# Performance work log

Hardware: AMD Instinct MI355X
Metric: run time of the kernel (lower is better)

## Reference

```python
import jax, jax.numpy as jnp
import numpy as np

WS = 8       # window_size
SHIFT = 4    # shift_size
HEADS = 4

def _rel_pos_index():
    coords = np.stack(np.meshgrid(np.arange(WS), np.arange(WS), indexing='ij'))
    cf = coords.reshape(2, -1)                       # (2, N)
    rel = cf[:, :, None] - cf[:, None, :]            # (2, N, N)
    rel = rel.transpose(1, 2, 0).copy()              # (N, N, 2)
    rel[:, :, 0] += WS - 1
    rel[:, :, 1] += WS - 1
    rel[:, :, 0] *= 2 * WS - 1
    return jnp.asarray(rel.sum(-1))                  # (N, N) int

REL_IDX = _rel_pos_index()

def _conv(x, w, groups=1, pad=0):
    return jax.lax.conv_general_dilated(
        x, w, (1, 1), [(pad, pad), (pad, pad)],
        feature_group_count=groups,
        dimension_numbers=('NCHW', 'OIHW', 'NCHW'))

def _dwt_haar(x):
    # single-level orthonormal Haar on non-overlapping 2x2 blocks
    B, C, H, W = x.shape
    x = x.reshape(B, C, H // 2, 2, W // 2, 2)
    a = x[:, :, :, 0, :, 0]; b = x[:, :, :, 0, :, 1]
    c = x[:, :, :, 1, :, 0]; d = x[:, :, :, 1, :, 1]
    ll = (a + b + c + d) * 0.5
    lh = (a - b + c - d) * 0.5
    hl = (a + b - c - d) * 0.5
    hh = (a - b - c + d) * 0.5
    return ll, lh, hl, hh

def _idwt_haar(ll, lh, hl, hh):
    a = (ll + lh + hl + hh) * 0.5
    b = (ll - lh + hl - hh) * 0.5
    c = (ll + lh - hl - hh) * 0.5
    d = (ll - lh - hl + hh) * 0.5
    B, C, H2, W2 = ll.shape
    x = jnp.stack([jnp.stack([a, b], -1), jnp.stack([c, d], -1)], -2)  # (B,C,H2,W2,2row,2col)
    return x.transpose(0, 1, 2, 4, 3, 5).reshape(B, C, 2 * H2, 2 * W2)

def _window_partition(x):
    B, C, H, W = x.shape
    x = x.reshape(B, C, H // WS, WS, W // WS, WS).transpose(0, 2, 4, 1, 3, 5)
    return x.reshape(-1, C, WS, WS)

def _window_reverse(w, B, H, W):
    C = w.shape[1]
    x = w.reshape(B, H // WS, W // WS, C, WS, WS).transpose(0, 3, 1, 4, 2, 5)
    return x.reshape(B, C, H, W)

def setup_inputs() -> dict:
    key = jax.random.key(0)
    ks = jax.random.split(key, 8)
    dim = 64
    s = 0.05
    return {
        'x': jax.random.normal(ks[0], (8, dim, 256, 256), jnp.float32),
        'temperature': jnp.ones((HEADS, 1, 1), jnp.float32),
        'rel_bias_table': jax.random.normal(ks[1], ((2 * WS - 1) ** 2, HEADS), jnp.float32) * 0.02,
        'w_high1': jax.random.normal(ks[2], (2 * dim, dim, 3, 3), jnp.float32) * s,
        'w_high2': jax.random.normal(ks[3], (dim, 2 * dim, 1, 1), jnp.float32) * s,
        'w_highout': jax.random.normal(ks[4], (3 * dim, dim, 3, 3), jnp.float32) * s,
        'w_qkv': jax.random.normal(ks[5], (3 * dim, dim, 1, 1), jnp.float32) * s,
        'w_dwconv': jax.random.normal(ks[6], (3 * dim, 1, 3, 3), jnp.float32) * s,
        'w_proj': jax.random.normal(ks[7], (dim, dim, 1, 1), jnp.float32) * s,
    }

def reference(x, temperature, rel_bias_table, w_high1, w_high2, w_highout, w_qkv, w_dwconv, w_proj):
    B, C, H, W = x.shape
    ll, lh, hl, hh = _dwt_haar(x)
    # high-frequency modulation of v
    filt = jax.nn.relu(_conv(jnp.concatenate([lh, hl], 1), w_high1, groups=2, pad=1))
    filt = jax.nn.relu(_conv(filt, w_high2))
    qkv = _conv(_conv(ll, w_qkv), w_dwconv, groups=3 * C, pad=1)
    v_inp = qkv[:, 2 * C:]  # note: q,k from qkv are dead in the source; q=k come from shifted LL
    v = v_inp * filt + v_inp
    xs = jnp.roll(ll, (-SHIFT, -SHIFT), (2, 3))
    qw = _window_partition(xs)
    vw = _window_partition(v)
    Bw = qw.shape[0]; hd = C // HEADS; N = WS * WS
    q = qw.reshape(Bw, HEADS, hd, N)
    vv = vw.reshape(Bw, HEADS, hd, N)
    qn = q / jnp.maximum(jnp.linalg.norm(q, axis=-2, keepdims=True), 1e-12)
    # k == q in the source, so kn == qn
    attn = jnp.einsum('bhdn,bhdm->bhnm', qn, qn)                      # (Bw,h,N,N)
    bias = rel_bias_table[REL_IDX.reshape(-1)].reshape(N, N, HEADS).transpose(2, 0, 1)
    attn = (attn + bias[None]) * temperature[None]
    attn = jax.nn.softmax(attn, axis=-1)
    out = jnp.einsum('bhdm,bhnm->bhdn', vv, attn)                     # v @ attn^T
    out = out.reshape(Bw, C, WS, WS)
    out = _window_reverse(out, B, H // 2, W // 2)
    out = jnp.roll(out, (SHIFT, SHIFT), (2, 3))
    out = _conv(out, w_proj)
    yh = jax.nn.relu(_conv(jnp.concatenate([lh, hl, hh], 1), w_highout, groups=3, pad=1))
    lh2, hl2, hh2 = yh[:, :C], yh[:, C:2 * C], yh[:, 2 * C:]
    return _idwt_haar(out, lh2, hl2, hh2)
```

## Files before the change

kernel.cpp:

```cpp
#include <hip/hip_runtime.h>
#include <cstddef>

constexpr int HP  = 128 * 128;
constexpr long long S = 8LL * 64 * HP;

using short8 = __attribute__((ext_vector_type(8))) short;
using f32x4  = __attribute__((ext_vector_type(4))) float;

__device__ __forceinline__ unsigned short f2bf(float x) {
    union { float f; unsigned int u; } v{x};
    unsigned int r = v.u + 0x7FFFu + ((v.u >> 16) & 1u);
    return (unsigned short)(r >> 16);
}

__global__ __launch_bounds__(256) void k_dwt(const float* __restrict__ x,
                                             float* __restrict__ ll, float* __restrict__ lh,
                                             float* __restrict__ hl, float* __restrict__ hh) {
    long long idx = (long long)blockIdx.x * 256 + threadIdx.x;
    if (idx >= S) return;
    int j  = (int)(idx & 127);
    int i  = (int)((idx >> 7) & 127);
    long long bc = idx >> 14;
    const float* xp = x + bc * 256 * 256;
    float2 top = *(const float2*)(xp + (2 * i) * 256 + 2 * j);
    float2 bot = *(const float2*)(xp + (2 * i + 1) * 256 + 2 * j);
    float a = top.x, b = top.y, c = bot.x, d = bot.y;
    ll[idx] = (a + b + c + d) * 0.5f;
    lh[idx] = (a - b + c - d) * 0.5f;
    hl[idx] = (a + b - c - d) * 0.5f;
    hh[idx] = (a - b - c + d) * 0.5f;
}

__global__ __launch_bounds__(256) void k_to_nhwc(const float* __restrict__ in,
                                                 unsigned short* __restrict__ out) {
    __shared__ float t[64][65];
    int b = blockIdx.y;
    int p0 = blockIdx.x * 64;
    int tid = threadIdx.x;
    const float* ib = in + (size_t)b * 64 * HP;
    {
        int p = tid & 63, c4 = tid >> 6;
#pragma unroll
        for (int k = 0; k < 16; ++k) {
            int c = c4 * 16 + k;
            t[c][p] = ib[(size_t)c * HP + p0 + p];
        }
    }
    __syncthreads();
    {
        int c = tid & 63, pq = tid >> 6;
        unsigned short* ob = out + ((size_t)b * HP + p0) * 64;
#pragma unroll
        for (int k = 0; k < 16; ++k) {
            int p = pq * 16 + k;
            ob[(size_t)p * 64 + c] = f2bf(t[c][p]);
        }
    }
}

__global__ __launch_bounds__(256) void k_wreorder(const float* __restrict__ w,
                                                  unsigned short* __restrict__ wr, int total) {
    int idx = blockIdx.x * 256 + threadIdx.x;
    if (idx >= total) return;
    int oc = idx / 576, rem = idx - oc * 576;
    int s = rem >> 6, ic = rem & 63;
    wr[idx] = f2bf(w[(oc * 64 + ic) * 9 + s]);
}

#define ISTR 72
__global__ __launch_bounds__(256, 2) void k_conv3x3_mfma(
        const unsigned short* __restrict__ in,
        const unsigned short* __restrict__ wr,
        float* __restrict__ out, int out_ctot) {
    __shared__ __align__(16) unsigned short lin[324 * ISTR];
    __shared__ __align__(16) unsigned short lw[64 * ISTR];

    int tid = threadIdx.x;
    int b = blockIdx.y;
    int ty0 = (blockIdx.x >> 3) * 16, tx0 = (blockIdx.x & 7) * 16;

    const unsigned short* inb = in + (size_t)b * HP * 64;
    for (int idx = tid; idx < 324 * 8; idx += 256) {
        int pr = idx >> 3, l8 = idx & 7;
        int py = pr / 18, px = pr - py * 18;
        int gy = ty0 + py - 1, gx = tx0 + px - 1;
        uint4 v = make_uint4(0, 0, 0, 0);
        if (gy >= 0 && gy < 128 && gx >= 0 && gx < 128)
            v = *(const uint4*)(inb + ((size_t)(gy * 128 + gx)) * 64 + l8 * 8);
        *(uint4*)&lin[pr * ISTR + l8 * 8] = v;
    }

    int wv = tid >> 6;
    int lane = tid & 63;
    int n16 = lane & 15, quad = lane >> 4;

    f32x4 acc[4][4];
#pragma unroll
    for (int mt = 0; mt < 4; ++mt)
#pragma unroll
        for (int nt = 0; nt < 4; ++nt) acc[mt][nt] = (f32x4){0.f, 0.f, 0.f, 0.f};

    for (int s = 0; s < 9; ++s) {
        __syncthreads();
        for (int idx = tid; idx < 512; idx += 256) {
            int oc = idx >> 3, l8 = idx & 7;
            *(uint4*)&lw[oc * ISTR + l8 * 8] =
                *(const uint4*)(wr + oc * 576 + s * 64 + l8 * 8);
        }
        __syncthreads();
        int sy = s / 3, sx = s - sy * 3;
#pragma unroll
        for (int half = 0; half < 2; ++half) {
            int ic0 = half * 32 + quad * 8;
            short8 a[4], bf[4];
#pragma unroll
            for (int mt = 0; mt < 4; ++mt)
                a[mt] = *(const short8*)&lw[(mt * 16 + n16) * ISTR + ic0];
#pragma unroll
            for (int nt = 0; nt < 4; ++nt) {
                int py = 4 * wv + nt + sy;
                int px = n16 + sx;
                bf[nt] = *(const short8*)&lin[(py * 18 + px) * ISTR + ic0];
            }
#pragma unroll
            for (int mt = 0; mt < 4; ++mt)
#pragma unroll
                for (int nt = 0; nt < 4; ++nt)
                    acc[mt][nt] = __builtin_amdgcn_mfma_f32_16x16x32_bf16(
                        a[mt], bf[nt], acc[mt][nt], 0, 0, 0);
        }
    }

    int gx = tx0 + n16;
#pragma unroll
    for (int nt = 0; nt < 4; ++nt) {
        int gy = ty0 + 4 * wv + nt;
#pragma unroll
        for (int mt = 0; mt < 4; ++mt) {
#pragma unroll
            for (int r = 0; r < 4; ++r) {
                int oc = mt * 16 + quad * 4 + r;
                out[((size_t)b * out_ctot + oc) * HP + (size_t)gy * 128 + gx] =
                    fmaxf(acc[mt][nt][r], 0.0f);
            }
        }
    }
}

template <int IC, bool RELU>
__global__ __launch_bounds__(256) void k_conv1x1(const float* __restrict__ in,
                                                 const float* __restrict__ w,
                                                 float* __restrict__ out) {
    __shared__ float wl[IC * 16];
    int tid = threadIdx.x;
    int occ = blockIdx.y, b = blockIdx.z;
    for (int idx = tid; idx < IC * 16; idx += 256) {
        int o = idx & 15, ic = idx >> 4;
        wl[idx] = w[(occ * 16 + o) * IC + ic];
    }
    __syncthreads();
    int p = blockIdx.x * 256 + tid;
    const float* inp = in + (size_t)b * IC * HP + p;
    float acc[16] = {};
    for (int ic = 0; ic < IC; ++ic) {
        float xv = inp[(size_t)ic * HP];
#pragma unroll
        for (int o = 0; o < 16; ++o) acc[o] += xv * wl[ic * 16 + o];
    }
    float* op = out + ((size_t)b * 64 + occ * 16) * HP + p;
#pragma unroll
    for (int o = 0; o < 16; ++o) op[o * HP] = RELU ? fmaxf(acc[o], 0.0f) : acc[o];
}

__global__ __launch_bounds__(256) void k_dwconv_v(const float* __restrict__ t,
                                                  const float* __restrict__ wdw,
                                                  const float* __restrict__ filt,
                                                  float* __restrict__ v) {
    long long idx = (long long)blockIdx.x * 256 + threadIdx.x;
    if (idx >= S) return;
    int j = (int)(idx & 127);
    int i = (int)((idx >> 7) & 127);
    int c = (int)((idx >> 14) & 63);
    long long bc = idx >> 14;
    const float* tp = t + bc * HP;
    const float* wp = wdw + c * 9;
    float acc = 0.0f;
#pragma unroll
    for (int ky = 0; ky < 3; ++ky) {
        int y = i + ky - 1;
        if (y < 0 || y >= 128) continue;
#pragma unroll
        for (int kx = 0; kx < 3; ++kx) {
            int x = j + kx - 1;
            if (x < 0 || x >= 128) continue;
            acc += tp[y * 128 + x] * wp[ky * 3 + kx];
        }
    }
    float f = filt[idx];
    v[idx] = acc * (1.0f + f);
}

__global__ __launch_bounds__(256) void k_attn(const float* __restrict__ ll,
                                              const float* __restrict__ v,
                                              const float* __restrict__ table,
                                              const float* __restrict__ temp,
                                              float* __restrict__ outbuf) {
    __shared__ float qs[64][64];
    __shared__ float vs[64][64];
    __shared__ float inv[4][64];
    __shared__ float tb[225 * 4];
    int blk = blockIdx.x;
    int wj = blk & 15, wi = (blk >> 4) & 15, b = blk >> 8;
    int tid = threadIdx.x;

    for (int idx = tid; idx < 900; idx += 256) tb[idx] = table[idx];
    for (int idx = tid; idx < 4096; idx += 256) {
        int c = idx >> 6, n = idx & 63;
        int i = n >> 3, j = n & 7;
        int qy = (wi * 8 + i + 4) & 127, qx = (wj * 8 + j + 4) & 127;
        int vy = wi * 8 + i, vx = wj * 8 + j;
        size_t cb = ((size_t)b * 64 + c) * HP;
        qs[c][n] = ll[cb + qy * 128 + qx];
        vs[c][n] = v[cb + vy * 128 + vx];
    }
    __syncthreads();

    int h = tid >> 6, n = tid & 63;
    float q[16];
    float ss = 0.0f;
#pragma unroll
    for (int d = 0; d < 16; ++d) {
        q[d] = qs[h * 16 + d][n];
        ss += q[d] * q[d];
    }
    float invn = 1.0f / fmaxf(sqrtf(ss), 1e-12f);
    inv[h][n] = invn;
    __syncthreads();

    int i1 = n >> 3, j1 = n & 7;
    float tscale = temp[h];
    float p[64];
    float mx = -1e30f;
#pragma unroll
    for (int m = 0; m < 64; ++m) {
        float s = 0.0f;
#pragma unroll
        for (int d = 0; d < 16; ++d) s += q[d] * qs[h * 16 + d][m];
        s = s * invn * inv[h][m];
        int i2 = m >> 3, j2 = m & 7;
        s += tb[((i1 - i2 + 7) * 15 + (j1 - j2 + 7)) * 4 + h];
        s *= tscale;
        p[m] = s;
        mx = fmaxf(mx, s);
    }
    float sum = 0.0f;
#pragma unroll
    for (int m = 0; m < 64; ++m) {
        p[m] = __expf(p[m] - mx);
        sum += p[m];
    }
    float rs = 1.0f / sum;
    float acc[16] = {};
#pragma unroll
    for (int m = 0; m < 64; ++m) {
        float pm = p[m] * rs;
#pragma unroll
        for (int d = 0; d < 16; ++d) acc[d] += pm * vs[h * 16 + d][m];
    }
    int oy = (wi * 8 + i1 + 4) & 127, ox = (wj * 8 + j1 + 4) & 127;
#pragma unroll
    for (int d = 0; d < 16; ++d)
        outbuf[((size_t)b * 64 + h * 16 + d) * HP + oy * 128 + ox] = acc[d];
}

__global__ __launch_bounds__(256) void k_idwt(const float* __restrict__ ll, const float* __restrict__ lh,
                                              const float* __restrict__ hl, const float* __restrict__ hh,
                                              float* __restrict__ out) {
    long long idx = (long long)blockIdx.x * 256 + threadIdx.x;
    if (idx >= S) return;
    int j = (int)(idx & 127);
    int i = (int)((idx >> 7) & 127);
    long long bc = idx >> 14;
    float L = ll[idx], A = lh[idx], B = hl[idx], D = hh[idx];
    float a = (L + A + B + D) * 0.5f;
    float b = (L - A + B - D) * 0.5f;
    float c = (L + A - B - D) * 0.5f;
    float d = (L - A - B + D) * 0.5f;
    float* op = out + bc * 256 * 256;
    *(float2*)(op + (2 * i) * 256 + 2 * j) = make_float2(a, b);
    *(float2*)(op + (2 * i + 1) * 256 + 2 * j) = make_float2(c, d);
}

extern "C" void kernel_launch(void* const* d_in, const int* in_sizes, int n_in,
                              void* d_out, int out_size, void* d_ws, size_t ws_size,
                              hipStream_t stream) {
    const float* x        = (const float*)d_in[0];
    const float* temp     = (const float*)d_in[1];
    const float* table    = (const float*)d_in[2];
    const float* w_high1  = (const float*)d_in[3];
    const float* w_high2  = (const float*)d_in[4];
    const float* w_highout= (const float*)d_in[5];
    const float* w_qkv    = (const float*)d_in[6];
    const float* w_dwconv = (const float*)d_in[7];
    const float* w_proj   = (const float*)d_in[8];
    float* out = (float*)d_out;

    float* ws = (float*)d_ws;
    float* s0 = ws + 0 * S;
    float* s1 = ws + 1 * S;
    float* s2 = ws + 2 * S;
    float* s3 = ws + 3 * S;
    float* s4 = ws + 4 * S;
    float* s5 = ws + 5 * S;
    float* s6 = ws + 6 * S;
    float* s7 = ws + 7 * S;
    float* s8 = ws + 8 * S;

    unsigned short* T_lh = (unsigned short*)s4;
    unsigned short* T_hl = (unsigned short*)s4 + S;
    unsigned short* T_hh = (unsigned short*)s5;
    unsigned short* w_r1 = (unsigned short*)s5 + S;
    unsigned short* w_r2 = w_r1 + 128 * 576;

    const int nblk = (int)(S / 256);
    dim3 b256(256);

    k_dwt<<<nblk, b256, 0, stream>>>(x, s0, s1, s2, s3);

    dim3 tg(HP / 64, 8);
    k_to_nhwc<<<tg, b256, 0, stream>>>(s1, T_lh);
    k_to_nhwc<<<tg, b256, 0, stream>>>(s2, T_hl);
    k_to_nhwc<<<tg, b256, 0, stream>>>(s3, T_hh);
    k_wreorder<<<(128 * 576 + 255) / 256, b256, 0, stream>>>(w_high1, w_r1, 128 * 576);
    k_wreorder<<<(192 * 576 + 255) / 256, b256, 0, stream>>>(w_highout, w_r2, 192 * 576);

    dim3 cg(64, 8);
    k_conv3x3_mfma<<<cg, b256, 0, stream>>>(T_lh, w_r1,            s1,            128);
    k_conv3x3_mfma<<<cg, b256, 0, stream>>>(T_hl, w_r1 + 64 * 576, s1 + 64 * HP,  128);

    dim3 g1(64, 4, 8);
    k_conv1x1<128, true><<<g1, b256, 0, stream>>>(s1, w_high2, s6);

    k_conv1x1<64, false><<<g1, b256, 0, stream>>>(s0, w_qkv + 128 * 64, s7);

    k_dwconv_v<<<nblk, b256, 0, stream>>>(s7, w_dwconv + 128 * 9, s6, s6);

    k_attn<<<2048, b256, 0, stream>>>(s0, s6, table, temp, s7);

    k_conv1x1<64, false><<<g1, b256, 0, stream>>>(s7, w_proj, s8);

    k_conv3x3_mfma<<<cg, b256, 0, stream>>>(T_lh, w_r2,             s1, 64);
    k_conv3x3_mfma<<<cg, b256, 0, stream>>>(T_hl, w_r2 + 64 * 576,  s2, 64);
    k_conv3x3_mfma<<<cg, b256, 0, stream>>>(T_hh, w_r2 + 128 * 576, s3, 64);

    k_idwt<<<nblk, b256, 0, stream>>>(s8, s1, s2, s3, out);
}
```

Before: 652.1 us.

## Fuse Haar DWT with NHWC bf16 transpose and tile attention with online softmax

Merges the DWT kernel with the three NHWC/bf16 transpose kernels, so the high-frequency subbands go straight into bf16 NHWC and the fp32 lh/hl/hh round-trips through global memory are gone. The attention kernel is restructured into 16-column chunks with an online softmax, float4 shared-memory reads and a precomputed scaled bias matrix built by a new small kernel. This drops the 64-element per-thread score array, lowering register pressure so launch bounds can ask for 4 blocks per SM. The costs are an extra tiny launch and some extra exp and rescale work per chunk.

```diff
diff --git a/kernel.cpp b/kernel.cpp
--- a/kernel.cpp
+++ b/kernel.cpp
@@ -13,47 +13,44 @@
     return (unsigned short)(r >> 16);
 }
 
-__global__ __launch_bounds__(256) void k_dwt(const float* __restrict__ x,
-                                             float* __restrict__ ll, float* __restrict__ lh,
-                                             float* __restrict__ hl, float* __restrict__ hh) {
-    long long idx = (long long)blockIdx.x * 256 + threadIdx.x;
-    if (idx >= S) return;
-    int j  = (int)(idx & 127);
-    int i  = (int)((idx >> 7) & 127);
-    long long bc = idx >> 14;
-    const float* xp = x + bc * 256 * 256;
-    float2 top = *(const float2*)(xp + (2 * i) * 256 + 2 * j);
-    float2 bot = *(const float2*)(xp + (2 * i + 1) * 256 + 2 * j);
-    float a = top.x, b = top.y, c = bot.x, d = bot.y;
-    ll[idx] = (a + b + c + d) * 0.5f;
-    lh[idx] = (a - b + c - d) * 0.5f;
-    hl[idx] = (a + b - c - d) * 0.5f;
-    hh[idx] = (a - b - c + d) * 0.5f;
-}
-
-__global__ __launch_bounds__(256) void k_to_nhwc(const float* __restrict__ in,
-                                                 unsigned short* __restrict__ out) {
-    __shared__ float t[64][65];
+__global__ __launch_bounds__(256) void k_dwt_fused(
+        const float* __restrict__ x, float* __restrict__ ll,
+        unsigned short* __restrict__ Tlh, unsigned short* __restrict__ Thl,
+        unsigned short* __restrict__ Thh) {
+    __shared__ unsigned short tlh[64][66];
+    __shared__ unsigned short thl[64][66];
+    __shared__ unsigned short thh[64][66];
     int b = blockIdx.y;
     int p0 = blockIdx.x * 64;
+    int i = p0 >> 7, j0 = p0 & 127;
     int tid = threadIdx.x;
-    const float* ib = in + (size_t)b * 64 * HP;
     {
         int p = tid & 63, c4 = tid >> 6;
+        int j = j0 + p;
+        const float* xb = x + (size_t)b * 64 * 65536;
 #pragma unroll
         for (int k = 0; k < 16; ++k) {
             int c = c4 * 16 + k;
-            t[c][p] = ib[(size_t)c * HP + p0 + p];
+            const float* xp = xb + (size_t)c * 65536;
+            float2 top = *(const float2*)(xp + (2 * i) * 256 + 2 * j);
+            float2 bot = *(const float2*)(xp + (2 * i + 1) * 256 + 2 * j);
+            float a = top.x, bb = top.y, cc = bot.x, dd = bot.y;
+            ll[((size_t)b * 64 + c) * HP + p0 + p] = (a + bb + cc + dd) * 0.5f;
+            tlh[c][p] = f2bf((a - bb + cc - dd) * 0.5f);
+            thl[c][p] = f2bf((a + bb - cc - dd) * 0.5f);
+            thh[c][p] = f2bf((a - bb - cc + dd) * 0.5f);
         }
     }
     __syncthreads();
     {
         int c = tid & 63, pq = tid >> 6;
-        unsigned short* ob = out + ((size_t)b * HP + p0) * 64;
+        size_t ob = ((size_t)b * HP + p0) * 64;
 #pragma unroll
         for (int k = 0; k < 16; ++k) {
             int p = pq * 16 + k;
-            ob[(size_t)p * 64 + c] = f2bf(t[c][p]);
+            Tlh[ob + (size_t)p * 64 + c] = tlh[c][p];
+            Thl[ob + (size_t)p * 64 + c] = thl[c][p];
+            Thh[ob + (size_t)p * 64 + c] = thh[c][p];
         }
     }
 }
@@ -65,6 +62,16 @@
     int oc = idx / 576, rem = idx - oc * 576;
     int s = rem >> 6, ic = rem & 63;
     wr[idx] = f2bf(w[(oc * 64 + ic) * 9 + s]);
+}
+
+__global__ __launch_bounds__(256) void k_bias(const float* __restrict__ table,
+                                              const float* __restrict__ temp,
+                                              float* __restrict__ bd) {
+    int idx = blockIdx.x * 256 + threadIdx.x;
+    int h = idx >> 12, m = (idx >> 6) & 63, n = idx & 63;
+    int i1 = n >> 3, j1 = n & 7, i2 = m >> 3, j2 = m & 7;
+    int rel = (i1 - i2 + 7) * 15 + (j1 - j2 + 7);
+    bd[idx] = table[rel * 4 + h] * temp[h];
 }
 
 #define ISTR 72
@@ -200,20 +207,20 @@
     v[idx] = acc * (1.0f + f);
 }
 
-__global__ __launch_bounds__(256) void k_attn(const float* __restrict__ ll,
-                                              const float* __restrict__ v,
-                                              const float* __restrict__ table,
-                                              const float* __restrict__ temp,
-                                              float* __restrict__ outbuf) {
-    __shared__ float qs[64][64];
-    __shared__ float vs[64][64];
-    __shared__ float inv[4][64];
-    __shared__ float tb[225 * 4];
+union F16 { float4 v4[4]; float f[16]; };
+
+__global__ __launch_bounds__(256, 4) void k_attn(const float* __restrict__ ll,
+                                                 const float* __restrict__ v,
+                                                 const float* __restrict__ bd,
+                                                 const float* __restrict__ temp,
+                                                 float* __restrict__ outbuf) {
+    __shared__ __align__(16) float qs[64][64];
+    __shared__ __align__(16) float vs[64][64];
+    __shared__ __align__(16) float inv[4][64];
     int blk = blockIdx.x;
     int wj = blk & 15, wi = (blk >> 4) & 15, b = blk >> 8;
     int tid = threadIdx.x;
 
-    for (int idx = tid; idx < 900; idx += 256) tb[idx] = table[idx];
     for (int idx = tid; idx < 4096; idx += 256) {
         int c = idx >> 6, n = idx & 63;
         int i = n >> 3, j = n & 7;
@@ -226,6 +233,7 @@
     __syncthreads();
 
     int h = tid >> 6, n = tid & 63;
+    float tscale = temp[h];
     float q[16];
     float ss = 0.0f;
 #pragma unroll
@@ -235,42 +243,70 @@
     }
     float invn = 1.0f / fmaxf(sqrtf(ss), 1e-12f);
     inv[h][n] = invn;
+    float qsc = invn * tscale;
+#pragma unroll
+    for (int d = 0; d < 16; ++d) q[d] *= qsc;
     __syncthreads();
 
+    const float* bh = bd + (h << 12) + n;
+    float mx = -1e30f, sum = 0.0f;
+    float acc[16] = {};
+
+    for (int c0 = 0; c0 < 64; c0 += 16) {
+        float bb[16];
+#pragma unroll
+        for (int mm = 0; mm < 16; ++mm) bb[mm] = bh[(c0 + mm) * 64];
+
+        float p[16] = {};
+#pragma unroll
+        for (int d = 0; d < 16; ++d) {
+            F16 A;
+            const float4* qr = (const float4*)&qs[h * 16 + d][c0];
+            A.v4[0] = qr[0]; A.v4[1] = qr[1]; A.v4[2] = qr[2]; A.v4[3] = qr[3];
+            float qd = q[d];
+#pragma unroll
+            for (int mm = 0; mm < 16; ++mm) p[mm] += qd * A.f[mm];
+        }
+        F16 I;
+        const float4* ir = (const float4*)&inv[h][c0];
+        I.v4[0] = ir[0]; I.v4[1] = ir[1]; I.v4[2] = ir[2]; I.v4[3] = ir[3];
+        float cm = -1e30f;
+#pragma unroll
+        for (int mm = 0; mm < 16; ++mm) {
+            p[mm] = p[mm] * I.f[mm] + bb[mm];
+            cm = fmaxf(cm, p[mm]);
+        }
+
+        float nm = fmaxf(mx, cm);
+        float scale = __expf(mx - nm);
+        sum *= scale;
+#pragma unroll
+        for (int mm = 0; mm < 16; ++mm) {
+            p[mm] = __expf(p[mm] - nm);
+            sum += p[mm];
+        }
+#pragma unroll
+        for (int d = 0; d < 16; ++d) acc[d] *= scale;
+
+#pragma unroll
+        for (int d = 0; d < 16; ++d) {
+            F16 V;
+            const float4* vr = (const float4*)&vs[h * 16 + d][c0];
+            V.v4[0] = vr[0]; V.v4[1] = vr[1]; V.v4[2] = vr[2]; V.v4[3] = vr[3];
+            float s = acc[d];
+#pragma unroll
+            for (int mm = 0; mm < 16; ++mm) s += p[mm] * V.f[mm];
+            acc[d] = s;
+        }
+        mx = nm;
+    }
+
+    float rs = 1.0f / sum;
     int i1 = n >> 3, j1 = n & 7;
-    float tscale = temp[h];
-    float p[64];
-    float mx = -1e30f;
-#pragma unroll
-    for (int m = 0; m < 64; ++m) {
-        float s = 0.0f;
-#pragma unroll
-        for (int d = 0; d < 16; ++d) s += q[d] * qs[h * 16 + d][m];
-        s = s * invn * inv[h][m];
-        int i2 = m >> 3, j2 = m & 7;
-        s += tb[((i1 - i2 + 7) * 15 + (j1 - j2 + 7)) * 4 + h];
-        s *= tscale;
-        p[m] = s;
-        mx = fmaxf(mx, s);
-    }
-    float sum = 0.0f;
-#pragma unroll
-    for (int m = 0; m < 64; ++m) {
-        p[m] = __expf(p[m] - mx);
-        sum += p[m];
-    }
-    float rs = 1.0f / sum;
-    float acc[16] = {};
-#pragma unroll
-    for (int m = 0; m < 64; ++m) {
-        float pm = p[m] * rs;
-#pragma unroll
-        for (int d = 0; d < 16; ++d) acc[d] += pm * vs[h * 16 + d][m];
-    }
     int oy = (wi * 8 + i1 + 4) & 127, ox = (wj * 8 + j1 + 4) & 127;
 #pragma unroll
     for (int d = 0; d < 16; ++d)
-        outbuf[((size_t)b * 64 + h * 16 + d) * HP + oy * 128 + ox] = acc[d];
+        outbuf[((size_t)b * 64 + h * 16 + d) * HP + oy * 128 + ox] = acc[d] * rs;
 }
 
 __global__ __launch_bounds__(256) void k_idwt(const float* __restrict__ ll, const float* __restrict__ lh,
@@ -321,18 +357,17 @@
     unsigned short* T_hh = (unsigned short*)s5;
     unsigned short* w_r1 = (unsigned short*)s5 + S;
     unsigned short* w_r2 = w_r1 + 128 * 576;
+    float* bd = (float*)(w_r2 + 192 * 576);
 
     const int nblk = (int)(S / 256);
     dim3 b256(256);
 
-    k_dwt<<<nblk, b256, 0, stream>>>(x, s0, s1, s2, s3);
-
-    dim3 tg(HP / 64, 8);
-    k_to_nhwc<<<tg, b256, 0, stream>>>(s1, T_lh);
-    k_to_nhwc<<<tg, b256, 0, stream>>>(s2, T_hl);
-    k_to_nhwc<<<tg, b256, 0, stream>>>(s3, T_hh);
+    dim3 dg(HP / 64, 8);
+    k_dwt_fused<<<dg, b256, 0, stream>>>(x, s0, T_lh, T_hl, T_hh);
+
     k_wreorder<<<(128 * 576 + 255) / 256, b256, 0, stream>>>(w_high1, w_r1, 128 * 576);
     k_wreorder<<<(192 * 576 + 255) / 256, b256, 0, stream>>>(w_highout, w_r2, 192 * 576);
+    k_bias<<<64, b256, 0, stream>>>(table, temp, bd);
 
     dim3 cg(64, 8);
     k_conv3x3_mfma<<<cg, b256, 0, stream>>>(T_lh, w_r1,            s1,            128);
@@ -345,7 +380,7 @@
 
     k_dwconv_v<<<nblk, b256, 0, stream>>>(s7, w_dwconv + 128 * 9, s6, s6);
 
-    k_attn<<<2048, b256, 0, stream>>>(s0, s6, table, temp, s7);
+    k_attn<<<2048, b256, 0, stream>>>(s0, s6, bd, temp, s7);
 
     k_conv1x1<64, false><<<g1, b256, 0, stream>>>(s7, w_proj, s8);
 
```

Result: faster. 618.4 us (-5.2%).
